# Kernel tuning notes

Hardware: AMD Instinct MI355X
Metric: run time of the kernel (lower is better)

The kernel has to match this reference:

```python
import jax, jax.numpy as jnp
import numpy as np

EPS = 1e-5

def conv(x, w, b=None, padding=0, groups=1, dilation=1):
    out = jax.lax.conv_general_dilated(
        x, w, window_strides=(1, 1), padding=[(padding, padding)] * 2,
        rhs_dilation=(dilation, dilation), feature_group_count=groups,
        dimension_numbers=('NCHW', 'OIHW', 'NCHW'))
    if b is not None:
        out = out + b[None, :, None, None]
    return out

def bn(x, g, b):
    # eval-mode BatchNorm with running_mean=0, running_var=1
    return x * (g / jnp.sqrt(1.0 + EPS))[None, :, None, None] + b[None, :, None, None]

def _gather_bilinear_corner(xf, yi, xi, H, W):
    # xf: [B, C, H*W]; yi/xi: [B, K2, H, W] int32 corner coords
    valid = (yi >= 0) & (yi < H) & (xi >= 0) & (xi < W)
    idx = jnp.clip(yi, 0, H - 1) * W + jnp.clip(xi, 0, W - 1)  # [B,K2,H,W]
    B = xf.shape[0]
    g = jax.vmap(lambda xb, ib: xb[:, ib])(xf, idx.reshape(B, -1))  # [B,C,K2*H*W]
    g = g.reshape(B, xf.shape[1], *yi.shape[1:])  # [B,C,K2,H,W]
    return g * valid[:, None].astype(xf.dtype)

def deform_dw_conv(x, offset, w_dw, pad, dil, kh=3, kw=3):
    # torchvision DeformConv2d, depthwise (groups=C), stride 1.
    # offset: [B, 2*kh*kw, H, W], ordering (dy, dx) per kernel tap.
    B, C, H, W = x.shape
    K2 = kh * kw
    off = offset.reshape(B, K2, 2, H, W)
    dy, dx = off[:, :, 0], off[:, :, 1]  # [B,K2,H,W]
    k = jnp.arange(K2)
    ky = ((k // kw) * dil - pad).astype(x.dtype)  # [K2]
    kx = ((k % kw) * dil - pad).astype(x.dtype)
    py = jnp.arange(H, dtype=x.dtype)[None, None, :, None] + ky[None, :, None, None] + dy
    px = jnp.arange(W, dtype=x.dtype)[None, None, None, :] + kx[None, :, None, None] + dx
    y0 = jnp.floor(py); x0 = jnp.floor(px)
    fy = py - y0; fx = px - x0
    y0i = y0.astype(jnp.int32); x0i = x0.astype(jnp.int32)
    y1i = y0i + 1; x1i = x0i + 1
    xf = x.reshape(B, C, H * W)
    v00 = _gather_bilinear_corner(xf, y0i, x0i, H, W)
    v01 = _gather_bilinear_corner(xf, y0i, x1i, H, W)
    v10 = _gather_bilinear_corner(xf, y1i, x0i, H, W)
    v11 = _gather_bilinear_corner(xf, y1i, x1i, H, W)
    fy = fy[:, None]; fx = fx[:, None]  # [B,1,K2,H,W]
    val = (v00 * (1 - fy) * (1 - fx) + v01 * (1 - fy) * fx
           + v10 * fy * (1 - fx) + v11 * fy * fx)  # [B,C,K2,H,W]
    return jnp.einsum('bckhw,ck->bchw', val, w_dw.reshape(C, K2))

def reference(x, w_conv1, g1, b1, w_off, b_off, w_dw, g_b, b_b,
              w_conv2, g2, b2, w_fc1, b_fc1, w_fc2, b_fc2):
    silu = jax.nn.silu
    h = silu(bn(conv(x, w_conv1), g1, b1))
    # MFC_Bottleneck (n=1): offset conv -> deform depthwise conv -> BN -> SiLU -> residual
    off = conv(h, w_off, b_off, padding=1)
    d = deform_dw_conv(h, off, w_dw, pad=1, dil=1)
    h = silu(bn(d, g_b, b_b)) + h
    y = silu(bn(conv(h, w_conv2), g2, b2))
    # SE block
    s = jnp.mean(y, axis=(2, 3), keepdims=True)
    s = silu(conv(s, w_fc1, b_fc1))
    s = jax.nn.sigmoid(conv(s, w_fc2, b_fc2))
    return y * s

def setup_inputs() -> dict:
    key = jax.random.key(0)
    ks = jax.random.split(key, 8)
    B, C1, C2, HID, H, W = 4, 512, 512, 256, 64, 64
    SQ = C2 // 16
    sc = 0.02
    return {
        'x': jax.random.normal(ks[0], (B, C1, H, W), jnp.float32),
        'w_conv1': jax.random.normal(ks[1], (HID, C1, 1, 1), jnp.float32) * sc,
        'g1': jnp.ones((HID,), jnp.float32),
        'b1': jnp.zeros((HID,), jnp.float32),
        'w_off': jax.random.normal(ks[2], (18, HID, 3, 3), jnp.float32) * sc,
        'b_off': jnp.zeros((18,), jnp.float32),
        'w_dw': jax.random.normal(ks[3], (HID, 1, 3, 3), jnp.float32) * sc,
        'g_b': jnp.ones((HID,), jnp.float32),
        'b_b': jnp.zeros((HID,), jnp.float32),
        'w_conv2': jax.random.normal(ks[4], (C2, HID, 1, 1), jnp.float32) * sc,
        'g2': jnp.ones((C2,), jnp.float32),
        'b2': jnp.zeros((C2,), jnp.float32),
        'w_fc1': jax.random.normal(ks[5], (SQ, C2, 1, 1), jnp.float32) * sc,
        'b_fc1': jnp.zeros((SQ,), jnp.float32),
        'w_fc2': jax.random.normal(ks[6], (C2, SQ, 1, 1), jnp.float32) * sc,
        'b_fc2': jnp.zeros((C2,), jnp.float32),
    }
```

## Files before the change

### kernel.cpp

```cpp
#include <hip/hip_runtime.h>

#define HW 4096
#define BN_RS 0.9999950000374998f

typedef __attribute__((ext_vector_type(8))) short  short8;
typedef __attribute__((ext_vector_type(8))) unsigned short ushort8;
typedef __attribute__((ext_vector_type(4))) float  f32x4;
typedef __attribute__((ext_vector_type(2), aligned(4))) float f32x2u;
typedef __attribute__((ext_vector_type(2), aligned(8))) float f32x2a;

__device__ __forceinline__ float silu_f(float v) { return v / (1.0f + __expf(-v)); }
__device__ __forceinline__ int clamp64(int v) { return v < 0 ? 0 : (v > 63 ? 63 : v); }
__device__ __forceinline__ unsigned short f2bf(float f) {
    union { float f; unsigned u; } v; v.f = f;
    unsigned r = v.u + 0x7fff + ((v.u >> 16) & 1);
    return (unsigned short)(r >> 16);
}

template<int CO, int CIN>
__global__ __launch_bounds__(256) void k_conv1x1_mfma(
    const float* __restrict__ X, const float* __restrict__ Wt,
    const float* __restrict__ gg, const float* __restrict__ bb,
    float* __restrict__ Y)
{
    const int b  = blockIdx.z;
    const int p0 = blockIdx.x * 64;
    const int c0 = blockIdx.y * 64;
    const int tid  = threadIdx.x;
    const int wave = tid >> 6, lane = tid & 63;
    const int wm = wave >> 1, wn = wave & 1;
    const int lrow = lane & 15, lkg = lane >> 4;

    __shared__ __align__(16) unsigned short As[64 * 40];
    __shared__ __align__(16) unsigned short Bs[64 * 40];

    const float* Xb = X + (size_t)b * CIN * HW;

    f32x4 acc[2][2];
    #pragma unroll
    for (int i = 0; i < 2; ++i)
        #pragma unroll
        for (int j = 0; j < 2; ++j) acc[i][j] = (f32x4){0.f, 0.f, 0.f, 0.f};

    const int arow = tid >> 2, akc = (tid & 3) * 8;

    for (int k0 = 0; k0 < CIN; k0 += 32) {
        __syncthreads();
        {
            const float* wp = &Wt[(size_t)(c0 + arow) * CIN + k0 + akc];
            float4 v0 = *(const float4*)wp;
            float4 v1 = *(const float4*)(wp + 4);
            ushort8 u;
            u[0] = f2bf(v0.x); u[1] = f2bf(v0.y); u[2] = f2bf(v0.z); u[3] = f2bf(v0.w);
            u[4] = f2bf(v1.x); u[5] = f2bf(v1.y); u[6] = f2bf(v1.z); u[7] = f2bf(v1.w);
            *(ushort8*)&As[arow * 40 + akc] = u;
        }
        #pragma unroll
        for (int it = 0; it < 2; ++it) {
            int i  = tid + it * 256;
            int kk = i >> 4;
            int p4 = (i & 15) * 4;
            float4 v = *(const float4*)&Xb[(size_t)(k0 + kk) * HW + p0 + p4];
            int kg = kk >> 3, kl = kk & 7;
            float vv[4] = {v.x, v.y, v.z, v.w};
            #pragma unroll
            for (int jj = 0; jj < 4; ++jj) {
                int pos = p4 + jj;
                int kgs = kg ^ ((pos >> 3) & 3);
                Bs[pos * 40 + kgs * 8 + kl] = f2bf(vv[jj]);
            }
        }
        __syncthreads();

        short8 aF[2], bF[2];
        #pragma unroll
        for (int mi = 0; mi < 2; ++mi)
            aF[mi] = *(const short8*)&As[(wm * 32 + mi * 16 + lrow) * 40 + lkg * 8];
        #pragma unroll
        for (int ni = 0; ni < 2; ++ni) {
            int pos = wn * 32 + ni * 16 + lrow;
            int kgs = lkg ^ ((pos >> 3) & 3);
            bF[ni] = *(const short8*)&Bs[pos * 40 + kgs * 8];
        }
        #pragma unroll
        for (int mi = 0; mi < 2; ++mi)
            #pragma unroll
            for (int ni = 0; ni < 2; ++ni)
                acc[mi][ni] = __builtin_amdgcn_mfma_f32_16x16x32_bf16(
                    aF[mi], bF[ni], acc[mi][ni], 0, 0, 0);
    }

    #pragma unroll
    for (int mi = 0; mi < 2; ++mi) {
        #pragma unroll
        for (int r = 0; r < 4; ++r) {
            int co = c0 + wm * 32 + mi * 16 + lkg * 4 + r;
            float s  = gg[co] * BN_RS;
            float bi = bb[co];
            size_t rowb = ((size_t)b * CO + co) * HW + p0 + wn * 32 + lrow;
            Y[rowb]      = silu_f(fmaf(acc[mi][0][r], s, bi));
            Y[rowb + 16] = silu_f(fmaf(acc[mi][1][r], s, bi));
        }
    }
}

__global__ __launch_bounds__(256) void k_woff_t(
    const float* __restrict__ Wo, unsigned short* __restrict__ Wt2)
{
    const int t = blockIdx.x;
    const int co = blockIdx.y;
    const int ci = threadIdx.x;
    float v = (co < 18) ? Wo[((size_t)co * 256 + ci) * 9 + t] : 0.0f;
    Wt2[((size_t)t * 32 + co) * 256 + ci] = f2bf(v);
}

__global__ __launch_bounds__(256) void k_conv_off(
    const float* __restrict__ Hh, const unsigned short* __restrict__ Wt2,
    float* __restrict__ OffP)
{
    const int y = blockIdx.x;
    const int b = blockIdx.y;
    const int q = blockIdx.z;
    const int tid = threadIdx.x;
    const int wn = tid >> 6;
    const int lane = tid & 63;
    const int lrow = lane & 15, lkg = lane >> 4;

    __shared__ __align__(16) unsigned short hsT[3][66][40];

    f32x4 acc[2];
    acc[0] = (f32x4){0.f, 0.f, 0.f, 0.f};
    acc[1] = (f32x4){0.f, 0.f, 0.f, 0.f};

    for (int cc = 0; cc < 2; ++cc) {
        const int ci0 = q * 64 + cc * 32;
        __syncthreads();
        if (tid < 192) {
            int r = tid / 64, which = (tid >> 5) & 1, ci = tid & 31;
            hsT[r][which ? 65 : 0][ci] = 0;
        }
        #pragma unroll
        for (int it = 0; it < 6; ++it) {
            int i  = tid + it * 256;
            int r  = i >> 9;
            int ci = (i >> 4) & 31;
            int x4 = (i & 15) << 2;
            int yy = y + r - 1;
            float4 v = make_float4(0.f, 0.f, 0.f, 0.f);
            if ((unsigned)yy < 64u)
                v = *(const float4*)&Hh[((size_t)(b * 256 + ci0 + ci) << 12) + yy * 64 + x4];
            hsT[r][1 + x4 + 0][ci] = f2bf(v.x);
            hsT[r][1 + x4 + 1][ci] = f2bf(v.y);
            hsT[r][1 + x4 + 2][ci] = f2bf(v.z);
            hsT[r][1 + x4 + 3][ci] = f2bf(v.w);
        }
        __syncthreads();

        #pragma unroll
        for (int t9 = 0; t9 < 9; ++t9) {
            const int ty = t9 / 3, tx = t9 % 3;
            short8 bF = *(const short8*)&hsT[ty][wn * 16 + lrow + tx][lkg * 8];
            #pragma unroll
            for (int mi = 0; mi < 2; ++mi) {
                short8 aF = *(const short8*)&Wt2[((size_t)t9 * 32 + mi * 16 + lrow) * 256
                                                 + ci0 + lkg * 8];
                acc[mi] = __builtin_amdgcn_mfma_f32_16x16x32_bf16(aF, bF, acc[mi], 0, 0, 0);
            }
        }
    }

    #pragma unroll
    for (int mi = 0; mi < 2; ++mi) {
        #pragma unroll
        for (int r = 0; r < 4; ++r) {
            int co = mi * 16 + lkg * 4 + r;
            if (co < 18)
                OffP[(((size_t)q * 4 + b) * 18 + co) * HW + y * 64 + wn * 16 + lrow]
                    = acc[mi][r];
        }
    }
}

__global__ __launch_bounds__(256) void k_off_combine(
    const float* __restrict__ OffP, const float* __restrict__ Bo,
    float* __restrict__ Off2)
{
    const int bk = blockIdx.x;
    const int b = bk / 9, k = bk - b * 9;
    const int t0 = 2 * k, t1 = 2 * k + 1;
    const float bias0 = Bo[t0], bias1 = Bo[t1];
    const size_t p0 = ((size_t)b * 18 + t0) * HW;
    const size_t p1 = ((size_t)b * 18 + t1) * HW;
    float* outp = Off2 + (((size_t)b * 9 + k) * HW) * 2;
    #pragma unroll
    for (int it = 0; it < 4; ++it) {
        int p4 = (threadIdx.x + it * 256) * 4;
        float4 s0 = *(const float4*)&OffP[p0 + p4];
        float4 s1 = *(const float4*)&OffP[p1 + p4];
        #pragma unroll
        for (int q = 1; q < 4; ++q) {
            float4 v0 = *(const float4*)&OffP[((size_t)q * 4 * 18) * HW + p0 + p4];
            float4 v1 = *(const float4*)&OffP[((size_t)q * 4 * 18) * HW + p1 + p4];
            s0.x += v0.x; s0.y += v0.y; s0.z += v0.z; s0.w += v0.w;
            s1.x += v1.x; s1.y += v1.y; s1.z += v1.z; s1.w += v1.w;
        }
        s0.x += bias0; s0.y += bias0; s0.z += bias0; s0.w += bias0;
        s1.x += bias1; s1.y += bias1; s1.z += bias1; s1.w += bias1;
        float4 o01 = make_float4(s0.x, s1.x, s0.y, s1.y);
        float4 o23 = make_float4(s0.z, s1.z, s0.w, s1.w);
        *(float4*)&outp[p4 * 2]     = o01;
        *(float4*)&outp[p4 * 2 + 4] = o23;
    }
}

__global__ __launch_bounds__(256) void k_deform(
    const float* __restrict__ Hh, const float* __restrict__ Off2,
    const float* __restrict__ Wd, const float* __restrict__ Gb,
    const float* __restrict__ Bb, float* __restrict__ H2)
{
    const int idx = blockIdx.x;
    const int bq  = idx & 31;
    const int y   = idx >> 5;
    const int b   = bq >> 3;
    const int q   = bq & 7;
    const int tid = threadIdx.x;
    const int x = tid & 63;
    const int g = tid >> 6;
    const int pos = y * 64 + x;

    __shared__ __align__(16) float hsw[5][32][68];
    __shared__ __align__(16) float wds[9 * 32];
    __shared__ float gbs[32], bbs[32];

    for (int i = tid; i < 288; i += 256) {
        int lc = i & 31, k = i >> 5;
        wds[i] = Wd[(q * 32 + lc) * 9 + k];
    }
    if (tid < 32) {
        gbs[tid] = Gb[q * 32 + tid] * BN_RS;
        bbs[tid] = Bb[q * 32 + tid];
    }

    int w0 = y - 2; w0 = w0 < 0 ? 0 : (w0 > 59 ? 59 : w0);
    const float* hq = Hh + ((size_t)(b * 256 + q * 32) << 12);
    #pragma unroll
    for (int it = 0; it < 10; ++it) {
        int i = tid + it * 256;
        int slot = i >> 9, ch = (i >> 4) & 31, x4 = (i & 15) << 2;
        float4 v = *(const float4*)&hq[((size_t)ch << 12) + (w0 + slot) * 64 + x4];
        *(float4*)&hsw[slot][ch][x4] = v;
    }
    __syncthreads();

    float acc[8];
    #pragma unroll
    for (int j = 0; j < 8; ++j) acc[j] = 0.f;

    const float* Ob   = Off2 + ((size_t)b * 9 * HW + pos) * 2;
    const float* hb0  = hq + ((size_t)(g * 8) << 12);
    const float* ldsb = &hsw[0][0][0];

    for (int r = 0; r < 3; ++r) {
        int   rb0[3], rb1[3], lb0[3], lb1[3];
        int   o0[3], o1[3];
        float wy0[3], wy1[3], wx0[3], wx1[3];
        bool inw = true;
        #pragma unroll
        for (int t = 0; t < 3; ++t) {
            int k = r * 3 + t;
            f32x2a dv = *(const f32x2a*)(Ob + (size_t)k * HW * 2);
            float dy = dv.x, dx = dv.y;
            float py = (float)(y + r - 1) + dy;
            float px = (float)(x + t - 1) + dx;
            float fy0 = floorf(py), fx0 = floorf(px);
            int y0 = (int)fy0, x0 = (int)fx0;
            float fy = py - fy0, fx = px - fx0;
            bool vy0 = ((unsigned)y0 < 64u), vy1 = ((unsigned)(y0 + 1) < 64u);
            bool vx0 = ((unsigned)x0 < 64u), vx1 = ((unsigned)(x0 + 1) < 64u);
            int cy0 = clamp64(y0), cy1 = clamp64(y0 + 1);
            int bx  = x0 < 0 ? 0 : (x0 > 62 ? 62 : x0);
            int d0 = x0 - bx;
            o0[t] = d0 < 0 ? 0 : d0;
            int d1 = d0 + 1;
            o1[t] = d1 > 1 ? 1 : d1;
            rb0[t] = cy0 * 64 + bx;
            rb1[t] = cy1 * 64 + bx;
            lb0[t] = (cy0 - w0) * 2176 + bx;
            lb1[t] = (cy1 - w0) * 2176 + bx;
            inw = inw && (cy0 >= w0) && (cy1 <= w0 + 4);
            wy0[t] = vy0 ? (1.0f - fy) : 0.0f;
            wy1[t] = vy1 ? fy : 0.0f;
            wx0[t] = vx0 ? (1.0f - fx) : 0.0f;
            wx1[t] = vx1 ? fx : 0.0f;
        }
        if (__all(inw)) {
            #pragma unroll
            for (int j = 0; j < 8; ++j) {
                const int chb = (g * 8 + j) * 68;
                float a = acc[j];
                #pragma unroll
                for (int t = 0; t < 3; ++t) {
                    f32x2u u0 = *(const f32x2u*)(ldsb + lb0[t] + chb);
                    f32x2u u1 = *(const f32x2u*)(ldsb + lb1[t] + chb);
                    float c00 = o0[t] ? u0.y : u0.x;
                    float c01 = o1[t] ? u0.y : u0.x;
                    float c10 = o0[t] ? u1.y : u1.x;
                    float c11 = o1[t] ? u1.y : u1.x;
                    float row0 = c00 * wx0[t] + c01 * wx1[t];
                    float row1 = c10 * wx0[t] + c11 * wx1[t];
                    float val  = row0 * wy0[t] + row1 * wy1[t];
                    a = fmaf(val, wds[(r * 3 + t) * 32 + g * 8 + j], a);
                }
                acc[j] = a;
            }
        } else {
            #pragma unroll
            for (int j = 0; j < 8; ++j) {
                const float* hb = hb0 + ((size_t)j << 12);
                float a = acc[j];
                #pragma unroll
                for (int t = 0; t < 3; ++t) {
                    f32x2u u0 = *(const f32x2u*)(hb + rb0[t]);
                    f32x2u u1 = *(const f32x2u*)(hb + rb1[t]);
                    float c00 = o0[t] ? u0.y : u0.x;
                    float c01 = o1[t] ? u0.y : u0.x;
                    float c10 = o0[t] ? u1.y : u1.x;
                    float c11 = o1[t] ? u1.y : u1.x;
                    float row0 = c00 * wx0[t] + c01 * wx1[t];
                    float row1 = c10 * wx0[t] + c11 * wx1[t];
                    float val  = row0 * wy0[t] + row1 * wy1[t];
                    a = fmaf(val, wds[(r * 3 + t) * 32 + g * 8 + j], a);
                }
                acc[j] = a;
            }
        }
    }

    const int ry = (y - w0) * 2176 + x;
    #pragma unroll
    for (int j = 0; j < 8; ++j) {
        int lc = g * 8 + j;
        float t = fmaf(acc[j], gbs[lc], bbs[lc]);
        float res = ldsb[ry + lc * 68];
        __builtin_nontemporal_store(silu_f(t) + res,
            &H2[((size_t)(b * 256 + q * 32 + lc) << 12) + pos]);
    }
}

__global__ __launch_bounds__(256) void k_se_reduce(
    const float* __restrict__ Y, float* __restrict__ sb)
{
    const int bc = blockIdx.x;
    const float4* p = (const float4*)(Y + (size_t)bc * HW);
    int tid = threadIdx.x;
    float s = 0.f;
    #pragma unroll
    for (int it = 0; it < 4; ++it) {
        float4 v = p[tid + it * 256];
        s += v.x + v.y + v.z + v.w;
    }
    #pragma unroll
    for (int o = 32; o > 0; o >>= 1) s += __shfl_down(s, o);
    __shared__ float red[4];
    if ((tid & 63) == 0) red[tid >> 6] = s;
    __syncthreads();
    if (tid == 0) sb[bc] = (red[0] + red[1] + red[2] + red[3]) * (1.0f / 4096.0f);
}

__global__ __launch_bounds__(256) void k_se_fc(
    const float* __restrict__ sb, const float* __restrict__ wf1,
    const float* __restrict__ bf1, const float* __restrict__ wf2,
    const float* __restrict__ bf2, float* __restrict__ s2)
{
    const int b = blockIdx.x;
    const int t = threadIdx.x;
    __shared__ float sv[512];
    __shared__ float s1[32];
    sv[t]       = sb[b * 512 + t];
    sv[t + 256] = sb[b * 512 + t + 256];
    __syncthreads();
    if (t < 32) {
        float a = bf1[t];
        const float* w = wf1 + t * 512;
        for (int i = 0; i < 512; ++i) a = fmaf(w[i], sv[i], a);
        s1[t] = silu_f(a);
    }
    __syncthreads();
    #pragma unroll
    for (int it = 0; it < 2; ++it) {
        int co = t + it * 256;
        float a = bf2[co];
        const float* w = wf2 + co * 32;
        #pragma unroll
        for (int i = 0; i < 32; ++i) a = fmaf(w[i], s1[i], a);
        s2[b * 512 + co] = 1.0f / (1.0f + __expf(-a));
    }
}

__global__ __launch_bounds__(256) void k_se_scale(
    float* __restrict__ Y, const float* __restrict__ s2)
{
    size_t i = (size_t)blockIdx.x * 256 + threadIdx.x;
    int bc = (int)(i >> 10);
    float sc = s2[bc];
    float4 v = ((float4*)Y)[i];
    v.x *= sc; v.y *= sc; v.z *= sc; v.w *= sc;
    ((float4*)Y)[i] = v;
}

extern "C" void kernel_launch(void* const* d_in, const int* in_sizes, int n_in,
                              void* d_out, int out_size, void* d_ws, size_t ws_size,
                              hipStream_t stream)
{
    const float* x   = (const float*)d_in[0];
    const float* w1  = (const float*)d_in[1];
    const float* g1  = (const float*)d_in[2];
    const float* b1  = (const float*)d_in[3];
    const float* wof = (const float*)d_in[4];
    const float* bof = (const float*)d_in[5];
    const float* wdw = (const float*)d_in[6];
    const float* gb  = (const float*)d_in[7];
    const float* bbv = (const float*)d_in[8];
    const float* w2  = (const float*)d_in[9];
    const float* g2  = (const float*)d_in[10];
    const float* b2  = (const float*)d_in[11];
    const float* wf1 = (const float*)d_in[12];
    const float* bf1 = (const float*)d_in[13];
    const float* wf2 = (const float*)d_in[14];
    const float* bf2 = (const float*)d_in[15];
    float* out = (float*)d_out;

    const size_t n_h    = 4ull * 256 * HW;
    const size_t n_offp = 4ull * 4 * 18 * HW;
    const size_t n_off  = 4ull * 18 * HW;
    const size_t n_wt2  = 9 * 32 * 256 / 2;
    float* ws = (float*)d_ws;
    float *h, *offp, *offc, *h2, *sb, *s2, *wt2f;
    size_t need = (2 * n_h + n_offp + n_off + 2048 + 2048 + n_wt2 + 1024) * sizeof(float);
    if (ws_size >= need) {
        h = ws; offp = h + n_h; offc = offp + n_offp; h2 = offc + n_off;
        sb = h2 + n_h; s2 = sb + 2048; wt2f = s2 + 2048;
    } else {
        h = out;
        offp = ws; offc = offp + n_offp; h2 = offc + n_off;
        sb = h2 + n_h; s2 = sb + 2048; wt2f = s2 + 2048;
    }
    unsigned short* wt2 = (unsigned short*)wt2f;

    k_conv1x1_mfma<256, 512><<<dim3(64, 4, 4), 256, 0, stream>>>(x, w1, g1, b1, h);
    k_woff_t<<<dim3(9, 32), 256, 0, stream>>>(wof, wt2);
    k_conv_off<<<dim3(64, 4, 4), 256, 0, stream>>>(h, wt2, offp);
    k_off_combine<<<36, 256, 0, stream>>>(offp, bof, offc);
    k_deform<<<2048, 256, 0, stream>>>(h, offc, wdw, gb, bbv, h2);
    k_conv1x1_mfma<512, 256><<<dim3(64, 8, 4), 256, 0, stream>>>(h2, w2, g2, b2, out);
    k_se_reduce<<<2048, 256, 0, stream>>>(out, sb);
    k_se_fc<<<4, 256, 0, stream>>>(sb, wf1, bf1, wf2, bf2, s2);
    k_se_scale<<<8192, 256, 0, stream>>>(out, s2);
}
```

Measured before the change: 138.3 us.

## Prefetch next K-tile into registers and swizzle block order in 1x1 conv GEMM

New measurement: 133.8 us. 1.03x faster.

```diff
diff --git a/kernel.cpp b/kernel.cpp
--- a/kernel.cpp
+++ b/kernel.cpp
@@ -16,6 +16,9 @@
     unsigned r = v.u + 0x7fff + ((v.u >> 16) & 1);
     return (unsigned short)(r >> 16);
 }
+__device__ __forceinline__ unsigned packbf(float lo, float hi) {
+    return (unsigned)f2bf(lo) | ((unsigned)f2bf(hi) << 16);
+}
 
 template<int CO, int CIN>
 __global__ __launch_bounds__(256) void k_conv1x1_mfma(
@@ -23,9 +26,16 @@
     const float* __restrict__ gg, const float* __restrict__ bb,
     float* __restrict__ Y)
 {
-    const int b  = blockIdx.z;
-    const int p0 = blockIdx.x * 64;
-    const int c0 = blockIdx.y * 64;
+    constexpr int NC = CO / 64;
+    const int id   = blockIdx.x;
+    const int low3 = id & 7;
+    const int rest = id >> 3;
+    const int c0i  = rest % NC;
+    const int tile = (rest / NC) * 8 + low3;
+    const int b  = tile >> 6;
+    const int p0 = (tile & 63) * 64;
+    const int c0 = c0i * 64;
+
     const int tid  = threadIdx.x;
     const int wave = tid >> 6, lane = tid & 63;
     const int wm = wave >> 1, wn = wave & 1;
@@ -43,34 +53,44 @@
         for (int j = 0; j < 2; ++j) acc[i][j] = (f32x4){0.f, 0.f, 0.f, 0.f};
 
     const int arow = tid >> 2, akc = (tid & 3) * 8;
-
+    const int kp = tid >> 4, p4 = (tid & 15) * 4;
+
+    ushort8 aP;
+    uint4   bP;
+
+    auto LOAD = [&](int k0) {
+        const float* wp = &Wt[(size_t)(c0 + arow) * CIN + k0 + akc];
+        float4 v0 = *(const float4*)wp;
+        float4 v1 = *(const float4*)(wp + 4);
+        ushort8 u;
+        u[0] = f2bf(v0.x); u[1] = f2bf(v0.y); u[2] = f2bf(v0.z); u[3] = f2bf(v0.w);
+        u[4] = f2bf(v1.x); u[5] = f2bf(v1.y); u[6] = f2bf(v1.z); u[7] = f2bf(v1.w);
+        aP = u;
+        const float* xp = &Xb[(size_t)(k0 + 2 * kp) * HW + p0 + p4];
+        float4 x0 = *(const float4*)xp;
+        float4 x1 = *(const float4*)(xp + HW);
+        bP.x = packbf(x0.x, x1.x);
+        bP.y = packbf(x0.y, x1.y);
+        bP.z = packbf(x0.z, x1.z);
+        bP.w = packbf(x0.w, x1.w);
+    };
+
+    LOAD(0);
     for (int k0 = 0; k0 < CIN; k0 += 32) {
         __syncthreads();
+        *(ushort8*)&As[arow * 40 + akc] = aP;
         {
-            const float* wp = &Wt[(size_t)(c0 + arow) * CIN + k0 + akc];
-            float4 v0 = *(const float4*)wp;
-            float4 v1 = *(const float4*)(wp + 4);
-            ushort8 u;
-            u[0] = f2bf(v0.x); u[1] = f2bf(v0.y); u[2] = f2bf(v0.z); u[3] = f2bf(v0.w);
-            u[4] = f2bf(v1.x); u[5] = f2bf(v1.y); u[6] = f2bf(v1.z); u[7] = f2bf(v1.w);
-            *(ushort8*)&As[arow * 40 + akc] = u;
-        }
-        #pragma unroll
-        for (int it = 0; it < 2; ++it) {
-            int i  = tid + it * 256;
-            int kk = i >> 4;
-            int p4 = (i & 15) * 4;
-            float4 v = *(const float4*)&Xb[(size_t)(k0 + kk) * HW + p0 + p4];
-            int kg = kk >> 3, kl = kk & 7;
-            float vv[4] = {v.x, v.y, v.z, v.w};
+            const int kg = kp >> 2, kl2 = (kp & 3) * 2;
+            const unsigned bw[4] = {bP.x, bP.y, bP.z, bP.w};
             #pragma unroll
             for (int jj = 0; jj < 4; ++jj) {
                 int pos = p4 + jj;
                 int kgs = kg ^ ((pos >> 3) & 3);
-                Bs[pos * 40 + kgs * 8 + kl] = f2bf(vv[jj]);
+                *(unsigned*)&Bs[pos * 40 + kgs * 8 + kl2] = bw[jj];
             }
         }
         __syncthreads();
+        if (k0 + 32 < CIN) LOAD(k0 + 32);
 
         short8 aF[2], bF[2];
         #pragma unroll
@@ -447,12 +467,12 @@
     }
     unsigned short* wt2 = (unsigned short*)wt2f;
 
-    k_conv1x1_mfma<256, 512><<<dim3(64, 4, 4), 256, 0, stream>>>(x, w1, g1, b1, h);
+    k_conv1x1_mfma<256, 512><<<1024, 256, 0, stream>>>(x, w1, g1, b1, h);
     k_woff_t<<<dim3(9, 32), 256, 0, stream>>>(wof, wt2);
     k_conv_off<<<dim3(64, 4, 4), 256, 0, stream>>>(h, wt2, offp);
     k_off_combine<<<36, 256, 0, stream>>>(offp, bof, offc);
     k_deform<<<2048, 256, 0, stream>>>(h, offc, wdw, gb, bbv, h2);
-    k_conv1x1_mfma<512, 256><<<dim3(64, 8, 4), 256, 0, stream>>>(h2, w2, g2, b2, out);
+    k_conv1x1_mfma<512, 256><<<2048, 256, 0, stream>>>(h2, w2, g2, b2, out);
     k_se_reduce<<<2048, 256, 0, stream>>>(out, sb);
     k_se_fc<<<4, 256, 0, stream>>>(sb, wf1, bf1, wf2, bf2, s2);
     k_se_scale<<<8192, 256, 0, stream>>>(out, s2);
```
